# Optimization experiments

Measured on AMD Instinct MI355X. Metric: run time of the kernel, lower is better.

## Reference

```python
import jax, jax.numpy as jnp
import numpy as np

K = 7                 # kernel_size = inhibition_kernel.shape[3]
PAD = 3               # hardcoded ReflectionPad2d((3,3,3,3))
MEMBRANE_DECAY = 0.99


def setup_inputs() -> dict:
    key = jax.random.key(0)
    k1, k2 = jax.random.split(key)
    B, C, H, W = 16, 16, 64, 64
    # spikes are binary events; sparse-ish activity
    in_spikes = (jax.random.uniform(k1, (B, C, H, W)) < 0.1).astype(jnp.float32)
    # weights: (out_h, out_w, C_in, k, k, C_out), init randn * 1/(k*k)
    weights = jax.random.normal(k2, (H, W, C, K, K, C), dtype=jnp.float32) * (1.0 / (K * K))
    membrane = jnp.ones((B, C, H, W), dtype=jnp.float32)
    return {"in_spikes": in_spikes, "weights": weights, "membrane": membrane}


def reference(in_spikes, weights, membrane):
    B, C, H, W = in_spikes.shape
    # ReflectionPad2d(3) on both spatial dims
    padded = jnp.pad(in_spikes, ((0, 0), (0, 0), (PAD, PAD), (PAD, PAD)), mode="reflect")
    # Extract all kxk patches (stride 1): fixed 49 shifted views -> (B, C, K, K, H, W)
    patches = jnp.stack(
        [padded[:, :, ki:ki + H, kj:kj + W] for ki in range(K) for kj in range(K)],
        axis=2,
    ).reshape(B, C, K, K, H, W)
    # Locally-connected (unshared weights) reduce over (c, ki, kj) per output location (i, j):
    # out[b, m, i, j] = sum_{c,x,y} patches[b, c, x, y, i, j] * weights[i, j, c, x, y, m]
    local = jnp.einsum("bcxyij,ijcxym->bmij", patches, weights)
    # LIF membrane/spike update
    mem = membrane * MEMBRANE_DECAY + local
    spike = (mem > 1).astype(in_spikes.dtype)
    mem = jnp.where(mem > 1, jnp.asarray(1.0, mem.dtype), mem)
    return spike, mem
```

## Files before the change

kernel.cpp:

```cpp
#include <hip/hip_runtime.h>

#define HW 64
#define NB 16
#define NC 16
#define KTOT 784
#define WPB 12544
#define CHUNK_K 128
#define CHUNK_F 2048

__device__ __forceinline__ int reflect64(int v) {
    if (v < 0) v = -v;
    if (v > 63) v = 126 - v;
    return v;
}

__global__ __launch_bounds__(256) void k_transpose(const float* __restrict__ in,
                                                   float* __restrict__ sT) {
    int gid = blockIdx.x * 256 + threadIdx.x;
    int b = gid & 15;
    int w = (gid >> 4) & 63;
    int h = (gid >> 10) & 63;
    int c = (gid >> 16) & 15;
    sT[gid] = in[b * 65536 + c * 4096 + h * 64 + w];
}

__global__ __launch_bounds__(256) void k_lc(const float* __restrict__ weights,
                                            const float* __restrict__ sT,
                                            float* __restrict__ oc) {
    __shared__ float buf[2][CHUNK_F];
    __shared__ __align__(16) unsigned table[KTOT];

    const int tid = threadIdx.x;
    const int bid = blockIdx.x;
    const int i = bid >> 6;
    const int j = bid & 63;

    if (tid < 196) {
#pragma unroll
        for (int e = 0; e < 4; ++e) {
            int k = tid * 4 + e;
            int c = (k * 1338) >> 16;
            int xy = k - c * 49;
            int x = (xy * 37) >> 8;
            int y = xy - x * 7;
            int r = reflect64(i + x - 3);
            int col = reflect64(j + y - 3);
            table[k] = (unsigned)(((c << 12) | (r << 6) | col) << 6);
        }
    }

    const int kp = tid >> 6;
    const int lane = tid & 63;
    const int m = lane >> 2;
    const int bq = lane & 3;
    const char* sTb = (const char*)sT + bq * 16;

    const float* Wg = weights + (size_t)bid * WPB;
    const float4* Wg4 = (const float4*)Wg;

    float4 acc = make_float4(0.f, 0.f, 0.f, 0.f);

    float4 s0 = Wg4[tid];
    float4 s1 = Wg4[tid + 256];
    float tailv = 0.f;

    for (int n = 0; n < 6; ++n) {
        __syncthreads();
        float4* bf4 = (float4*)(&buf[n & 1][0]);
        bf4[tid] = s0;
        bf4[tid + 256] = s1;
        if (n < 5) {
            s0 = Wg4[(n + 1) * 512 + tid];
            s1 = Wg4[(n + 1) * 512 + 256 + tid];
        } else {
            tailv = Wg[12288 + tid];
        }
        __syncthreads();

        const float* wb = &buf[n & 1][0];
        const int kb = n * CHUNK_K + kp * 32;
        const int kl = kp * 32;
#pragma unroll
        for (int g = 0; g < 8; ++g) {
            uint4 offs = *(const uint4*)&table[kb + g * 4];
            unsigned oarr[4] = {offs.x, offs.y, offs.z, offs.w};
#pragma unroll
            for (int q = 0; q < 4; ++q) {
                float4 s4 = *(const float4*)(sTb + oarr[q]);
                float w = wb[(kl + g * 4 + q) * 16 + m];
                acc.x += s4.x * w;
                acc.y += s4.y * w;
                acc.z += s4.z * w;
                acc.w += s4.w * w;
            }
        }
    }

    __syncthreads();
    buf[0][tid] = tailv;
    __syncthreads();
    {
        const float* wb = &buf[0][0];
        const int kb = 768 + kp * 4;
        const int kl = kp * 4;
        uint4 offs = *(const uint4*)&table[kb];
        unsigned oarr[4] = {offs.x, offs.y, offs.z, offs.w};
#pragma unroll
        for (int q = 0; q < 4; ++q) {
            float4 s4 = *(const float4*)(sTb + oarr[q]);
            float w = wb[(kl + q) * 16 + m];
            acc.x += s4.x * w;
            acc.y += s4.y * w;
            acc.z += s4.z * w;
            acc.w += s4.w * w;
        }
    }

    __syncthreads();
    float4* scr = (float4*)&buf[0][0];
    scr[kp * 64 + lane] = acc;
    __syncthreads();

    const int b = tid >> 4;
    const int mm = tid & 15;
    const int lane_src = mm * 4 + (b >> 2);
    const int d = b & 3;
    float sum = 0.f;
#pragma unroll
    for (int p = 0; p < 4; ++p) {
        float4 v = scr[p * 64 + lane_src];
        float vd = (d == 0) ? v.x : (d == 1) ? v.y : (d == 2) ? v.z : v.w;
        sum += vd;
    }
    oc[(size_t)bid * 256 + tid] = sum;
}

__global__ __launch_bounds__(256) void k_lif(const float* __restrict__ oc,
                                             const float* __restrict__ membrane,
                                             float* __restrict__ out) {
    __shared__ float tile[64][65];
    const int tb = blockIdx.x;
    const int ij0 = (tb >> 2) * 64;
    const int bm0 = (tb & 3) * 64;
    const int t = threadIdx.x;
    const int r0 = t >> 6;
    const int cl = t & 63;

#pragma unroll
    for (int p = 0; p < 16; ++p) {
        int ijl = p * 4 + r0;
        tile[ijl][cl] = oc[(size_t)(ij0 + ijl) * 256 + bm0 + cl];
    }
    __syncthreads();
#pragma unroll
    for (int p = 0; p < 16; ++p) {
        int bml = p * 4 + r0;
        int ijl = cl;
        float local = tile[ijl][bml];
        size_t idx = (size_t)(bm0 + bml) * 4096 + (ij0 + ijl);
        float memv = membrane[idx] * 0.99f + local;
        float spk = (memv > 1.0f) ? 1.0f : 0.0f;
        float mo = (memv > 1.0f) ? 1.0f : memv;
        out[idx] = spk;
        out[idx + 1048576] = mo;
    }
}

extern "C" void kernel_launch(void* const* d_in, const int* in_sizes, int n_in,
                              void* d_out, int out_size, void* d_ws, size_t ws_size,
                              hipStream_t stream) {
    const float* spikes = (const float*)d_in[0];
    const float* weights = (const float*)d_in[1];
    const float* membrane = (const float*)d_in[2];
    float* out = (float*)d_out;

    float* sT = (float*)d_ws;
    float* oc = (float*)d_ws + (1 << 20);

    k_transpose<<<4096, 256, 0, stream>>>(spikes, sT);
    k_lc<<<4096, 256, 0, stream>>>(weights, sT, oc);
    k_lif<<<256, 256, 0, stream>>>(oc, membrane, out);
}
```

Baseline: 360.1 us.

## Stage spikes and weights via direct global-to-LDS loads with triple buffering

The locally-connected kernel now gathers the reflected spike patches into shared memory up front with global_load_lds, then reads them from LDS instead of through an offset table from global memory. Weights stream through a three-deep LDS ring using asynchronous direct-to-LDS loads with manual waitcnt and barrier control, replacing register-staged double buffering. The transpose kernel is rewritten to use a shared tile for coalesced reads and writes. The change adds about 58KB of LDS per block, which may reduce occupancy, and depends on hand-managed vmcnt counts being correct.

```diff
diff --git a/kernel.cpp b/kernel.cpp
--- a/kernel.cpp
+++ b/kernel.cpp
@@ -1,136 +1,137 @@
 #include <hip/hip_runtime.h>
 
 #define HW 64
-#define NB 16
-#define NC 16
 #define KTOT 784
-#define WPB 12544
-#define CHUNK_K 128
-#define CHUNK_F 2048
+#define WPB_BYTES 50176u
+#define W_TOTAL_BYTES (4096u * WPB_BYTES)
+#define WEND (W_TOTAL_BYTES - 16u)
 
-__device__ __forceinline__ int reflect64(int v) {
-    if (v < 0) v = -v;
-    if (v > 63) v = 126 - v;
-    return v;
+__device__ __forceinline__ void gl16(const void* g, void* l) {
+    __builtin_amdgcn_global_load_lds(
+        (const __attribute__((address_space(1))) unsigned int*)g,
+        (__attribute__((address_space(3))) unsigned int*)l, 16, 0, 0);
 }
 
 __global__ __launch_bounds__(256) void k_transpose(const float* __restrict__ in,
                                                    float* __restrict__ sT) {
-    int gid = blockIdx.x * 256 + threadIdx.x;
-    int b = gid & 15;
-    int w = (gid >> 4) & 63;
-    int h = (gid >> 10) & 63;
-    int c = (gid >> 16) & 15;
-    sT[gid] = in[b * 65536 + c * 4096 + h * 64 + w];
+    __shared__ float tile[16][66];
+    const int c = blockIdx.x >> 6;
+    const int h = blockIdx.x & 63;
+    const int t = threadIdx.x;
+    const int wid = t >> 6, l = t & 63;
+#pragma unroll
+    for (int p = 0; p < 4; ++p) {
+        int b = p * 4 + wid;
+        tile[b][l] = in[((b << 4) + c) * 4096 + (h << 6) + l];
+    }
+    __syncthreads();
+    const int base = ((c << 6) | h) << 10;
+#pragma unroll
+    for (int p = 0; p < 4; ++p) {
+        int idx = p * 256 + t;
+        sT[base + idx] = tile[idx & 15][idx >> 4];
+    }
 }
 
 __global__ __launch_bounds__(256) void k_lc(const float* __restrict__ weights,
                                             const float* __restrict__ sT,
                                             float* __restrict__ oc) {
-    __shared__ float buf[2][CHUNK_F];
-    __shared__ __align__(16) unsigned table[KTOT];
+    __shared__ __align__(16) float s_spk[12544];
+    __shared__ __align__(16) float s_w[3][2048];
+    __shared__ __align__(16) float s_red[1024];
 
     const int tid = threadIdx.x;
     const int bid = blockIdx.x;
-    const int i = bid >> 6;
-    const int j = bid & 63;
+    const int i = bid >> 6, j = bid & 63;
+    const int wid = tid >> 6, lane = tid & 63;
+    const int m = lane >> 2, bq = lane & 3;
 
-    if (tid < 196) {
+    const char* wbase = (const char*)weights;
+    const char* sbase = (const char*)sT;
+    const unsigned wblk = (unsigned)bid * WPB_BYTES;
+
+    for (int s = wid; s < 49; s += 4) {
+        int k = s * 16 + (lane >> 2);
+        int c = (k * 1338) >> 16;
+        int xy = k - c * 49;
+        int x = (xy * 37) >> 8;
+        int y = xy - x * 7;
+        int r = i + x - 3; r = r < 0 ? -r : r; r = r > 63 ? 126 - r : r;
+        int q = j + y - 3; q = q < 0 ? -q : q; q = q > 63 ? 126 - q : q;
+        unsigned off = (unsigned)(((c << 12) | (r << 6) | q) << 6)
+                     + (unsigned)((lane & 3) << 4);
+        gl16(sbase + off, (char*)s_spk + s * 1024);
+    }
 #pragma unroll
-        for (int e = 0; e < 4; ++e) {
-            int k = tid * 4 + e;
-            int c = (k * 1338) >> 16;
-            int xy = k - c * 49;
-            int x = (xy * 37) >> 8;
-            int y = xy - x * 7;
-            int r = reflect64(i + x - 3);
-            int col = reflect64(j + y - 3);
-            table[k] = (unsigned)(((c << 12) | (r << 6) | col) << 6);
+    for (int nn = 0; nn < 3; ++nn) {
+#pragma unroll
+        for (int L = 0; L < 2; ++L) {
+            unsigned off = wblk + (unsigned)nn * 8192u
+                         + (unsigned)((L * 4 + wid) << 10) + (unsigned)(lane << 4);
+            off = off > WEND ? WEND : off;
+            gl16(wbase + off, (char*)&s_w[nn][0] + ((L * 4 + wid) << 10));
         }
     }
-
-    const int kp = tid >> 6;
-    const int lane = tid & 63;
-    const int m = lane >> 2;
-    const int bq = lane & 3;
-    const char* sTb = (const char*)sT + bq * 16;
-
-    const float* Wg = weights + (size_t)bid * WPB;
-    const float4* Wg4 = (const float4*)Wg;
+    asm volatile("s_waitcnt vmcnt(0)" ::: "memory");
+    __builtin_amdgcn_s_barrier();
 
     float4 acc = make_float4(0.f, 0.f, 0.f, 0.f);
-
-    float4 s0 = Wg4[tid];
-    float4 s1 = Wg4[tid + 256];
-    float tailv = 0.f;
-
+    int nb = 0;
     for (int n = 0; n < 6; ++n) {
-        __syncthreads();
-        float4* bf4 = (float4*)(&buf[n & 1][0]);
-        bf4[tid] = s0;
-        bf4[tid + 256] = s1;
-        if (n < 5) {
-            s0 = Wg4[(n + 1) * 512 + tid];
-            s1 = Wg4[(n + 1) * 512 + 256 + tid];
-        } else {
-            tailv = Wg[12288 + tid];
+        const float* wb = &s_w[nb][0] + wid * 512 + m;
+        const float4* sp = (const float4*)s_spk + (((n << 7) + (wid << 5)) << 2) + bq;
+#pragma unroll
+        for (int t = 0; t < 32; ++t) {
+            float4 s4 = sp[t * 4];
+            float w = wb[t * 16];
+            acc.x += s4.x * w; acc.y += s4.y * w;
+            acc.z += s4.z * w; acc.w += s4.w * w;
         }
-        __syncthreads();
-
-        const float* wb = &buf[n & 1][0];
-        const int kb = n * CHUNK_K + kp * 32;
-        const int kl = kp * 32;
+        asm volatile("s_waitcnt lgkmcnt(0)" ::: "memory");
+        __builtin_amdgcn_s_barrier();
+        {
+            const int nc = n + 3;
 #pragma unroll
-        for (int g = 0; g < 8; ++g) {
-            uint4 offs = *(const uint4*)&table[kb + g * 4];
-            unsigned oarr[4] = {offs.x, offs.y, offs.z, offs.w};
+            for (int L = 0; L < 2; ++L) {
+                unsigned off;
+                if (nc <= 6) {
+                    off = wblk + (unsigned)nc * 8192u
+                        + (unsigned)((L * 4 + wid) << 10) + (unsigned)(lane << 4);
+                    off = off > WEND ? WEND : off;
+                } else {
+                    off = WEND;
+                }
+                gl16(wbase + off, (char*)&s_w[nb][0] + ((L * 4 + wid) << 10));
+            }
+        }
+        asm volatile("s_waitcnt vmcnt(4)" ::: "memory");
+        __builtin_amdgcn_s_barrier();
+        nb = nb + 1; if (nb == 3) nb = 0;
+    }
+    {
+        const float* wb = &s_w[0][0] + wid * 64 + m;
+        const float4* sp = (const float4*)s_spk + ((768 + (wid << 2)) << 2) + bq;
 #pragma unroll
-            for (int q = 0; q < 4; ++q) {
-                float4 s4 = *(const float4*)(sTb + oarr[q]);
-                float w = wb[(kl + g * 4 + q) * 16 + m];
-                acc.x += s4.x * w;
-                acc.y += s4.y * w;
-                acc.z += s4.z * w;
-                acc.w += s4.w * w;
-            }
+        for (int t = 0; t < 4; ++t) {
+            float4 s4 = sp[t * 4];
+            float w = wb[t * 16];
+            acc.x += s4.x * w; acc.y += s4.y * w;
+            acc.z += s4.z * w; acc.w += s4.w * w;
         }
     }
 
     __syncthreads();
-    buf[0][tid] = tailv;
+    float4* scr = (float4*)s_red;
+    scr[wid * 64 + lane] = acc;
     __syncthreads();
-    {
-        const float* wb = &buf[0][0];
-        const int kb = 768 + kp * 4;
-        const int kl = kp * 4;
-        uint4 offs = *(const uint4*)&table[kb];
-        unsigned oarr[4] = {offs.x, offs.y, offs.z, offs.w};
-#pragma unroll
-        for (int q = 0; q < 4; ++q) {
-            float4 s4 = *(const float4*)(sTb + oarr[q]);
-            float w = wb[(kl + q) * 16 + m];
-            acc.x += s4.x * w;
-            acc.y += s4.y * w;
-            acc.z += s4.z * w;
-            acc.w += s4.w * w;
-        }
-    }
-
-    __syncthreads();
-    float4* scr = (float4*)&buf[0][0];
-    scr[kp * 64 + lane] = acc;
-    __syncthreads();
-
-    const int b = tid >> 4;
-    const int mm = tid & 15;
+    const int b = tid >> 4, mm = tid & 15;
     const int lane_src = mm * 4 + (b >> 2);
     const int d = b & 3;
     float sum = 0.f;
 #pragma unroll
     for (int p = 0; p < 4; ++p) {
         float4 v = scr[p * 64 + lane_src];
-        float vd = (d == 0) ? v.x : (d == 1) ? v.y : (d == 2) ? v.z : v.w;
-        sum += vd;
+        sum += (d == 0) ? v.x : (d == 1) ? v.y : (d == 2) ? v.z : v.w;
     }
     oc[(size_t)bid * 256 + tid] = sum;
 }
@@ -177,7 +178,7 @@
     float* sT = (float*)d_ws;
     float* oc = (float*)d_ws + (1 << 20);
 
-    k_transpose<<<4096, 256, 0, stream>>>(spikes, sT);
+    k_transpose<<<1024, 256, 0, stream>>>(spikes, sT);
     k_lc<<<4096, 256, 0, stream>>>(weights, sT, oc);
     k_lif<<<256, 256, 0, stream>>>(oc, membrane, out);
 }
```

New measurement: 306.0 us. 15.0% less time.
